# Kernel tuning notes

Measured on AMD Instinct MI355X. Metric: run time of the kernel, lower is better.

Reference implementation:

```python
import jax, jax.numpy as jnp
import numpy as np

DIM = 768
ALL_KEY_DIM = 768
NUM_HEADS = 12
HEAD_DIM = DIM // NUM_HEADS
SCALE = HEAD_DIM ** -0.5


def setup_inputs() -> dict:
    key = jax.random.key(0)
    ks = jax.random.split(key, 8)
    B, N = 8, 1024
    s = 0.02
    return {
        "x": jax.random.normal(ks[0], (B, N, DIM), dtype=jnp.float32),
        "Wq": jax.random.normal(ks[1], (ALL_KEY_DIM, DIM), dtype=jnp.float32) * s,
        "Wk": jax.random.normal(ks[2], (ALL_KEY_DIM, DIM), dtype=jnp.float32) * s,
        "Wv": jax.random.normal(ks[3], (DIM, DIM), dtype=jnp.float32) * s,
        "bv": jnp.zeros((DIM,), dtype=jnp.float32),
        "Wmix": jax.random.normal(ks[4], (NUM_HEADS, ALL_KEY_DIM), dtype=jnp.float32) * s,
        "Wcb": jax.random.normal(ks[5], (NUM_HEADS, DIM), dtype=jnp.float32) * s,
        "Wproj": jax.random.normal(ks[6], (DIM, DIM), dtype=jnp.float32) * s,
        "bproj": jnp.zeros((DIM,), dtype=jnp.float32),
    }


def reference(x, Wq, Wk, Wv, bv, Wmix, Wcb, Wproj, bproj):
    B, N, C = x.shape
    H, Dh = NUM_HEADS, C // NUM_HEADS
    q_shared = x @ Wq.T                      # [B,N,Dk]
    k = x @ Wk.T                             # [B,N,Dk]
    v = (x @ Wv.T + bv).reshape(B, N, H, Dh).transpose(0, 2, 1, 3)  # [B,H,N,Dh]
    # per-head mixed query: q[b,h,n,d] = q_shared[b,n,d] * Wmix[h,d]
    q = jnp.einsum('bnd,hd->bhnd', q_shared, Wmix)
    # shared-key scores + content bias broadcast over query positions
    scores = jnp.einsum('bhnd,bmd->bhnm', q, k)          # [B,H,N,N]
    content_bias = jnp.einsum('bmd,hd->bhm', x, Wcb)     # [B,H,N]
    attn = jax.nn.softmax((scores + content_bias[:, :, None, :]) * SCALE, axis=-1)
    out = jnp.einsum('bhnm,bhmd->bhnd', attn, v)         # [B,H,N,Dh]
    out = out.transpose(0, 2, 1, 3).reshape(B, N, C)
    return out @ Wproj.T + bproj
```

## Files before the change

### kernel.cpp

```cpp
#include <hip/hip_runtime.h>
#include <stdint.h>

typedef unsigned short u16;
typedef unsigned char u8;
typedef unsigned long long u64;
typedef __attribute__((ext_vector_type(8))) short bf16x8;
typedef __attribute__((ext_vector_type(4))) float f32x4;
typedef __attribute__((ext_vector_type(16))) float f32x16;

#define KLOG2E 0.18033688011112043f
#define QSCL 184.66496523378732f
#define SINV 0.0001220703125f
#define EXP2F(x) __builtin_amdgcn_exp2f(x)
#define WAITV(n) asm volatile("s_waitcnt vmcnt(" #n ")" ::: "memory")

__device__ __forceinline__ u16 f2bf(float f) {
  union { float f; unsigned u; } v; v.f = f;
  unsigned r = v.u + 0x7fffu + ((v.u >> 16) & 1u);
  return (u16)(r >> 16);
}
__device__ __forceinline__ float bf2f(u16 u) {
  union { unsigned u; float f; } v; v.u = ((unsigned)u) << 16;
  return v.f;
}
__device__ __forceinline__ u8 f2fp8(float f) {
  return (u8)(__builtin_amdgcn_cvt_pk_fp8_f32(f, f, 0, false) & 0xFF);
}

__device__ __forceinline__ void gload16(const void* g, void* l) {
  __builtin_amdgcn_global_load_lds(
      (const __attribute__((address_space(1))) unsigned int*)g,
      (__attribute__((address_space(3))) unsigned int*)l, 16, 0, 0);
}

__global__ void cvt_f32_bf16(const float4* __restrict__ s, uint2* __restrict__ d, int n4) {
  int i = blockIdx.x * blockDim.x + threadIdx.x;
  int stride = gridDim.x * blockDim.x;
  for (; i < n4; i += stride) {
    float4 v = s[i];
    uint2 o;
    o.x = (unsigned)f2bf(v.x) | ((unsigned)f2bf(v.y) << 16);
    o.y = (unsigned)f2bf(v.z) | ((unsigned)f2bf(v.w) << 16);
    d[i] = o;
  }
}

template <int MODE>
__global__ __launch_bounds__(256, 2) void gemm_bt(
    const u16* __restrict__ A, const u16* __restrict__ Bm,
    void* __restrict__ Cp, void* __restrict__ Cp2,
    const float* __restrict__ bias, int ldc) {
  __shared__ u16 Ab[128 * 32];
  __shared__ u16 Bb[128 * 32];
  const int tid = threadIdx.x;
  const int l = tid & 63, w = tid >> 6;
  const int g = l >> 4, l15 = l & 15;
  const int wr = w >> 1, wc = w & 1;
  const int rowbase = blockIdx.y * 128, colbase = blockIdx.x * 128;

  f32x4 acc[4][4] = {};
  const char* Abase = (const char*)A + (size_t)rowbase * 1536;
  const char* Bbase = (const char*)Bm + (size_t)colbase * 1536;

  for (int kk = 0; kk < 768; kk += 32) {
    __syncthreads();
#pragma unroll
    for (int p = 0; p < 2; ++p) {
      int o = p * 4096 + w * 1024 + l * 16;
      int row = o >> 6, cb = o & 63;
      gload16(Abase + (size_t)row * 1536 + kk * 2 + cb, &Ab[(p * 4096 + w * 1024) / 2]);
      gload16(Bbase + (size_t)row * 1536 + kk * 2 + cb, &Bb[(p * 4096 + w * 1024) / 2]);
    }
    __syncthreads();
    bf16x8 af[4], bfr[4];
#pragma unroll
    for (int i = 0; i < 4; ++i) {
      af[i] = *(const bf16x8*)&Ab[(wr * 64 + i * 16 + l15) * 32 + g * 8];
      bfr[i] = *(const bf16x8*)&Bb[(wc * 64 + i * 16 + l15) * 32 + g * 8];
    }
#pragma unroll
    for (int mi = 0; mi < 4; ++mi)
#pragma unroll
      for (int ni = 0; ni < 4; ++ni)
        acc[mi][ni] = __builtin_amdgcn_mfma_f32_16x16x32_bf16(af[mi], bfr[ni], acc[mi][ni], 0, 0, 0);
  }

#pragma unroll
  for (int mi = 0; mi < 4; ++mi)
#pragma unroll
    for (int ni = 0; ni < 4; ++ni)
#pragma unroll
      for (int r = 0; r < 4; ++r) {
        int row = rowbase + wr * 64 + mi * 16 + g * 4 + r;
        int col = colbase + wc * 64 + ni * 16 + l15;
        float v = acc[mi][ni][r];
        if (MODE == 0) {
          if (col < 768) {
            ((u16*)Cp)[(size_t)row * 768 + col] = f2bf(v);
          } else {
            int d = col - 768;
            int dp = d ^ ((((row) >> 3) & 1) << 3);
            ((u8*)Cp2)[(size_t)row * 768 + dp] = f2fp8(v * 8.0f);
          }
        } else if (MODE == 2) {
          ((float*)Cp)[(size_t)row * ldc + col] = v + bias[col];
        } else {
          int b = col >> 10, nn = col & 1023;
          if (row < 768) {
            ((u16*)Cp)[(size_t)b * 786432 + (size_t)row * 1024 + nn] = f2bf(v + bias[row]);
          } else if (row < 780) {
            ((float*)Cp2)[(size_t)b * 12288 + (size_t)(row - 768) * 1024 + nn] = v * KLOG2E;
          }
        }
      }
}

__global__ __launch_bounds__(256, 2) void attn10(
    const u16* __restrict__ Qb,
    const u8* __restrict__ Kf8,
    const u16* __restrict__ vT,
    const float* __restrict__ cb,
    const float* __restrict__ Wmix,
    u16* __restrict__ OH)
{
  __shared__ u8 Kb[3][8192];
  __shared__ u16 Vb[2][4096];
  __shared__ float cbL[1024];

  const int gid = blockIdx.x;
  const int b = gid & 7;
  const int within = gid >> 3;
  const int h = within % 12, qt = within / 12;
  const int tid = threadIdx.x;
  const int lane = tid & 63, w = tid >> 6;
  const int c = lane & 31, hi = lane >> 5;
  const int hsw = (c >> 3) & 1;

  const u8* Ksrc = Kf8 + (size_t)b * 786432;
  const char* Vsrc = (const char*)vT + (size_t)(b * 12 + h) * 131072;
  const float* cbp = cb + (size_t)(b * 12 + h) * 1024;

  long qreg[48];
  {
    const u16* qrow = Qb + ((size_t)b * 1024 + qt * 128 + w * 32 + c) * 768;
    const float* wmh = Wmix + h * 768;
#pragma unroll
    for (int D = 0; D < 48; ++D) {
      int off = D * 16 + hi * 8;
      bf16x8 qv = *(const bf16x8*)(qrow + off);
      float4 w0 = *(const float4*)(wmh + off);
      float4 w1 = *(const float4*)(wmh + off + 4);
      float q0 = bf2f((u16)qv[0]) * (w0.x * QSCL);
      float q1 = bf2f((u16)qv[1]) * (w0.y * QSCL);
      float q2 = bf2f((u16)qv[2]) * (w0.z * QSCL);
      float q3 = bf2f((u16)qv[3]) * (w0.w * QSCL);
      float q4 = bf2f((u16)qv[4]) * (w1.x * QSCL);
      float q5 = bf2f((u16)qv[5]) * (w1.y * QSCL);
      float q6 = bf2f((u16)qv[6]) * (w1.z * QSCL);
      float q7 = bf2f((u16)qv[7]) * (w1.w * QSCL);
      int a = __builtin_amdgcn_cvt_pk_fp8_f32(q0, q1, 0, false);
      a = __builtin_amdgcn_cvt_pk_fp8_f32(q2, q3, a, true);
      int b2 = __builtin_amdgcn_cvt_pk_fp8_f32(q4, q5, 0, false);
      b2 = __builtin_amdgcn_cvt_pk_fp8_f32(q6, q7, b2, true);
      qreg[D] = (long)(((u64)(unsigned)b2 << 32) | (u64)(unsigned)a);
    }
  }

  auto STK = [&](int kt2, int ch2, int buf) {
#pragma unroll
    for (int p4 = 0; p4 < 2; ++p4) {
      int o = p4 * 4096 + tid * 16;
      int row = o >> 7, t = (o >> 4) & 7;
      gload16(Ksrc + (size_t)(kt2 * 64 + row) * 768 + ch2 * 128 + ((t ^ (row & 7)) * 16),
              (char*)Kb[buf] + o);
    }
  };
  auto STV = [&](int kt2, int buf) {
#pragma unroll
    for (int p4 = 0; p4 < 2; ++p4) {
      int o = p4 * 4096 + tid * 16;
      int row = o >> 7, t = (o >> 4) & 7;
      gload16(Vsrc + (size_t)row * 2048 + kt2 * 128 + ((t ^ (row & 7)) * 16),
              (char*)Vb[buf] + o);
    }
  };

  {
    int o = tid * 16;
    gload16((const char*)cbp + o, (char*)cbL + o);
  }
  STK(0, 0, 0);
  STK(0, 1, 1);
  STV(0, 0);
  WAITV(0);
  __builtin_amdgcn_s_barrier();

  float m_run = -1e30f, lpart = 0.f;
  f32x16 oac0 = {}, oac1 = {};

#pragma unroll 1
  for (int kt = 0; kt < 16; ++kt) {
    f32x16 sa0 = {}, sa1 = {};
#pragma unroll
    for (int ch = 0; ch < 6; ++ch) {
      if (ch == 1 && kt < 15) STV(kt + 1, (kt + 1) & 1);
      if (ch <= 3) STK(kt, ch + 2, (ch + 2) % 3);
      else if (kt < 15) STK(kt + 1, ch - 4, (ch + 2) % 3);

      __builtin_amdgcn_s_setprio(1);
      const u8* kb0 = Kb[ch % 3] + c * 128 + ((hi ^ hsw) * 8);
#pragma unroll
      for (int s = 0; s < 8; ++s) {
        const u8* pK = kb0 + ((s ^ (c & 7)) << 4);
        long k0 = *(const long*)pK;
        long k1 = *(const long*)(pK + 4096);
        sa0 = __builtin_amdgcn_mfma_f32_32x32x16_fp8_fp8(k0, qreg[ch * 8 + s], sa0, 0, 0, 0);
        sa1 = __builtin_amdgcn_mfma_f32_32x32x16_fp8_fp8(k1, qreg[ch * 8 + s], sa1, 0, 0, 0);
      }
      __builtin_amdgcn_s_setprio(0);

      if (ch == 0) { WAITV(2); }
      else if (ch == 1) { if (kt < 15) { WAITV(4); } else { WAITV(2); } }
      else if (ch == 4 || ch == 5) { if (kt < 15) { WAITV(2); } else { WAITV(0); } }
      else { WAITV(2); }
      __builtin_amdgcn_s_barrier();
    }

    float cb0[16], cb1[16];
#pragma unroll
    for (int j = 0; j < 4; ++j) {
      float4 t0 = *(const float4*)&cbL[kt * 64 + 8 * j + 4 * hi];
      float4 t1 = *(const float4*)&cbL[kt * 64 + 32 + 8 * j + 4 * hi];
      cb0[4 * j] = t0.x; cb0[4 * j + 1] = t0.y; cb0[4 * j + 2] = t0.z; cb0[4 * j + 3] = t0.w;
      cb1[4 * j] = t1.x; cb1[4 * j + 1] = t1.y; cb1[4 * j + 2] = t1.z; cb1[4 * j + 3] = t1.w;
    }
    float pmax = -1e30f;
#pragma unroll
    for (int u = 0; u < 16; ++u) {
      sa0[u] = fmaf(sa0[u], SINV, cb0[u]);
      sa1[u] = fmaf(sa1[u], SINV, cb1[u]);
      pmax = fmaxf(pmax, fmaxf(sa0[u], sa1[u]));
    }
    pmax = fmaxf(pmax, __shfl_xor(pmax, 32));
    if (__ballot(pmax > m_run)) {
      float mnew = fmaxf(m_run, pmax);
      float alpha = EXP2F(m_run - mnew);
      lpart *= alpha;
      oac0 *= alpha;
      oac1 *= alpha;
      m_run = mnew;
    }
    float rs = 0.f;
#pragma unroll
    for (int u = 0; u < 16; ++u) {
      sa0[u] = EXP2F(sa0[u] - m_run); rs += sa0[u];
      sa1[u] = EXP2F(sa1[u] - m_run); rs += sa1[u];
    }
    rs += __shfl_xor(rs, 32);
    lpart += rs;

    const char* vb = (const char*)Vb[kt & 1];
#pragma unroll
    for (int kg = 0; kg < 2; ++kg) {
#pragma unroll
      for (int win = 0; win < 2; ++win) {
        float p0, p1, p2, p3, p4, p5, p6, p7;
        if (kg == 0) {
          p0 = sa0[win * 8 + 0]; p1 = sa0[win * 8 + 1]; p2 = sa0[win * 8 + 2]; p3 = sa0[win * 8 + 3];
          p4 = sa0[win * 8 + 4]; p5 = sa0[win * 8 + 5]; p6 = sa0[win * 8 + 6]; p7 = sa0[win * 8 + 7];
        } else {
          p0 = sa1[win * 8 + 0]; p1 = sa1[win * 8 + 1]; p2 = sa1[win * 8 + 2]; p3 = sa1[win * 8 + 3];
          p4 = sa1[win * 8 + 4]; p5 = sa1[win * 8 + 5]; p6 = sa1[win * 8 + 6]; p7 = sa1[win * 8 + 7];
        }
        unsigned xw, yw, zw, tw;
        asm("v_cvt_pk_bf16_f32 %0, %1, %2" : "=v"(xw) : "v"(p0), "v"(p1));
        asm("v_cvt_pk_bf16_f32 %0, %1, %2" : "=v"(yw) : "v"(p2), "v"(p3));
        asm("v_cvt_pk_bf16_f32 %0, %1, %2" : "=v"(zw) : "v"(p4), "v"(p5));
        asm("v_cvt_pk_bf16_f32 %0, %1, %2" : "=v"(tw) : "v"(p6), "v"(p7));
        asm volatile("v_permlane32_swap_b32 %0, %1" : "+v"(xw), "+v"(zw));
        asm volatile("v_permlane32_swap_b32 %0, %1" : "+v"(yw), "+v"(tw));
        union { unsigned u[4]; bf16x8 v; } bu;
        bu.u[0] = xw; bu.u[1] = yw; bu.u[2] = zw; bu.u[3] = tw;
#pragma unroll
        for (int dg = 0; dg < 2; ++dg) {
          int rd = dg * 32 + c;
          int sv = kg * 4 + win * 2 + hi;
          bf16x8 vf = *(const bf16x8*)(vb + rd * 128 + ((sv ^ (rd & 7)) * 16));
          if (dg == 0)
            oac0 = __builtin_amdgcn_mfma_f32_32x32x16_bf16(vf, bu.v, oac0, 0, 0, 0);
          else
            oac1 = __builtin_amdgcn_mfma_f32_32x32x16_bf16(vf, bu.v, oac1, 0, 0, 0);
        }
      }
    }
  }

  float rdiv = 1.f / lpart;
  int n = qt * 128 + w * 32 + c;
  size_t nrow = ((size_t)b * 1024 + n) * 768 + h * 64;
#pragma unroll
  for (int dg = 0; dg < 2; ++dg)
#pragma unroll
    for (int j = 0; j < 4; ++j) {
      f32x16 oo = dg == 0 ? oac0 : oac1;
      u64 pk = (u64)f2bf(oo[4 * j + 0] * rdiv) |
               ((u64)f2bf(oo[4 * j + 1] * rdiv) << 16) |
               ((u64)f2bf(oo[4 * j + 2] * rdiv) << 32) |
               ((u64)f2bf(oo[4 * j + 3] * rdiv) << 48);
      *(u64*)&OH[nrow + dg * 32 + 8 * j + 4 * hi] = pk;
    }
}

static inline int cvtblocks(int n4) {
  int nb = (n4 + 255) / 256;
  return nb > 2048 ? 2048 : nb;
}

extern "C" void kernel_launch(void* const* d_in, const int* in_sizes, int n_in,
                              void* d_out, int out_size, void* d_ws, size_t ws_size,
                              hipStream_t stream) {
  (void)in_sizes; (void)n_in; (void)out_size; (void)ws_size;
  const float* x = (const float*)d_in[0];
  const float* Wq = (const float*)d_in[1];
  const float* Wk = (const float*)d_in[2];
  const float* Wv = (const float*)d_in[3];
  const float* bv = (const float*)d_in[4];
  const float* Wmix = (const float*)d_in[5];
  const float* Wcb = (const float*)d_in[6];
  const float* Wproj = (const float*)d_in[7];
  const float* bproj = (const float*)d_in[8];
  float* out = (float*)d_out;

  char* ws = (char*)d_ws;
  u16* xbf = (u16*)(ws);
  u16* Wqk = (u16*)(ws + 12582912);
  u16* Wvcb = (u16*)(ws + 14942208);
  u16* Wpj = (u16*)(ws + 16318464);
  u16* Qb = (u16*)(ws + 17498112);
  u8* Kf8 = (u8*)(ws + 30081024);
  u16* vT = (u16*)(ws + 36372480);
  float* cbb = (float*)(ws + 48955392);
  u16* OH = (u16*)(ws + 49348608);

  cvt_f32_bf16<<<cvtblocks(1572864), 256, 0, stream>>>((const float4*)x, (uint2*)xbf, 1572864);
  cvt_f32_bf16<<<cvtblocks(147456), 256, 0, stream>>>((const float4*)Wq, (uint2*)Wqk, 147456);
  cvt_f32_bf16<<<cvtblocks(147456), 256, 0, stream>>>((const float4*)Wk, (uint2*)(Wqk + 589824), 147456);
  cvt_f32_bf16<<<cvtblocks(147456), 256, 0, stream>>>((const float4*)Wv, (uint2*)Wvcb, 147456);
  cvt_f32_bf16<<<cvtblocks(2304), 256, 0, stream>>>((const float4*)Wcb, (uint2*)(Wvcb + 589824), 2304);
  cvt_f32_bf16<<<cvtblocks(147456), 256, 0, stream>>>((const float4*)Wproj, (uint2*)Wpj, 147456);

  gemm_bt<0><<<dim3(12, 64), 256, 0, stream>>>(xbf, Wqk, Qb, Kf8, nullptr, 0);
  gemm_bt<1><<<dim3(64, 7), 256, 0, stream>>>(Wvcb, xbf, vT, cbb, bv, 0);
  attn10<<<dim3(768), 256, 0, stream>>>(Qb, Kf8, vT, cbb, Wmix, OH);
  gemm_bt<2><<<dim3(6, 64), 256, 0, stream>>>(OH, Wpj, out, nullptr, bproj, 768);
}
```

Before: 279.6 us.

## Use 32x32x64 scaled FP8 MFMA for QK scores with double-buffered 256-byte K chunks

Replaces the 32x32x16 fp8 MFMA in the QK^T score loop with the gfx950 mfma_scale 32x32x64 f8f6f4 instruction, so each instruction covers four times the reduction depth. K staging moves from a triple buffer of 128-byte-wide chunks to a double buffer of 256-byte chunks with a new XOR swizzle. Query packing becomes i32x8 registers, and Q preparation is moved after the first K/V loads are issued so it overlaps them. The K layout swizzle in the projection GEMM epilogue is dropped. Waits now sit before each compute step rather than after it, which exposes more load latency with only two buffers.

```diff
diff --git a/kernel.cpp b/kernel.cpp
--- a/kernel.cpp
+++ b/kernel.cpp
@@ -7,6 +7,7 @@
 typedef __attribute__((ext_vector_type(8))) short bf16x8;
 typedef __attribute__((ext_vector_type(4))) float f32x4;
 typedef __attribute__((ext_vector_type(16))) float f32x16;
+typedef __attribute__((ext_vector_type(8))) int i32x8;
 
 #define KLOG2E 0.18033688011112043f
 #define QSCL 184.66496523378732f
@@ -98,9 +99,7 @@
           if (col < 768) {
             ((u16*)Cp)[(size_t)row * 768 + col] = f2bf(v);
           } else {
-            int d = col - 768;
-            int dp = d ^ ((((row) >> 3) & 1) << 3);
-            ((u8*)Cp2)[(size_t)row * 768 + dp] = f2fp8(v * 8.0f);
+            ((u8*)Cp2)[(size_t)row * 768 + (col - 768)] = f2fp8(v * 8.0f);
           }
         } else if (MODE == 2) {
           ((float*)Cp)[(size_t)row * ldc + col] = v + bias[col];
@@ -115,7 +114,7 @@
       }
 }
 
-__global__ __launch_bounds__(256, 2) void attn10(
+__global__ __launch_bounds__(256, 2) void attn11(
     const u16* __restrict__ Qb,
     const u8* __restrict__ Kf8,
     const u16* __restrict__ vT,
@@ -123,7 +122,7 @@
     const float* __restrict__ Wmix,
     u16* __restrict__ OH)
 {
-  __shared__ u8 Kb[3][8192];
+  __shared__ u8 Kb[2][16384];
   __shared__ u16 Vb[2][4096];
   __shared__ float cbL[1024];
 
@@ -134,44 +133,18 @@
   const int tid = threadIdx.x;
   const int lane = tid & 63, w = tid >> 6;
   const int c = lane & 31, hi = lane >> 5;
-  const int hsw = (c >> 3) & 1;
 
   const u8* Ksrc = Kf8 + (size_t)b * 786432;
   const char* Vsrc = (const char*)vT + (size_t)(b * 12 + h) * 131072;
   const float* cbp = cb + (size_t)(b * 12 + h) * 1024;
 
-  long qreg[48];
-  {
-    const u16* qrow = Qb + ((size_t)b * 1024 + qt * 128 + w * 32 + c) * 768;
-    const float* wmh = Wmix + h * 768;
-#pragma unroll
-    for (int D = 0; D < 48; ++D) {
-      int off = D * 16 + hi * 8;
-      bf16x8 qv = *(const bf16x8*)(qrow + off);
-      float4 w0 = *(const float4*)(wmh + off);
-      float4 w1 = *(const float4*)(wmh + off + 4);
-      float q0 = bf2f((u16)qv[0]) * (w0.x * QSCL);
-      float q1 = bf2f((u16)qv[1]) * (w0.y * QSCL);
-      float q2 = bf2f((u16)qv[2]) * (w0.z * QSCL);
-      float q3 = bf2f((u16)qv[3]) * (w0.w * QSCL);
-      float q4 = bf2f((u16)qv[4]) * (w1.x * QSCL);
-      float q5 = bf2f((u16)qv[5]) * (w1.y * QSCL);
-      float q6 = bf2f((u16)qv[6]) * (w1.z * QSCL);
-      float q7 = bf2f((u16)qv[7]) * (w1.w * QSCL);
-      int a = __builtin_amdgcn_cvt_pk_fp8_f32(q0, q1, 0, false);
-      a = __builtin_amdgcn_cvt_pk_fp8_f32(q2, q3, a, true);
-      int b2 = __builtin_amdgcn_cvt_pk_fp8_f32(q4, q5, 0, false);
-      b2 = __builtin_amdgcn_cvt_pk_fp8_f32(q6, q7, b2, true);
-      qreg[D] = (long)(((u64)(unsigned)b2 << 32) | (u64)(unsigned)a);
-    }
-  }
-
-  auto STK = [&](int kt2, int ch2, int buf) {
-#pragma unroll
-    for (int p4 = 0; p4 < 2; ++p4) {
+  auto STK = [&](int kt2, int p2, int buf) {
+#pragma unroll
+    for (int p4 = 0; p4 < 4; ++p4) {
       int o = p4 * 4096 + tid * 16;
-      int row = o >> 7, t = (o >> 4) & 7;
-      gload16(Ksrc + (size_t)(kt2 * 64 + row) * 768 + ch2 * 128 + ((t ^ (row & 7)) * 16),
+      int row = o >> 8;
+      int t = (o >> 4) & 15;
+      gload16(Ksrc + (size_t)(kt2 * 64 + row) * 768 + p2 * 256 + ((t ^ (row & 15)) * 16),
               (char*)Kb[buf] + o);
     }
   };
@@ -190,10 +163,39 @@
     gload16((const char*)cbp + o, (char*)cbL + o);
   }
   STK(0, 0, 0);
-  STK(0, 1, 1);
   STV(0, 0);
-  WAITV(0);
-  __builtin_amdgcn_s_barrier();
+
+  i32x8 qreg[12];
+  {
+    const u16* qrow = Qb + ((size_t)b * 1024 + qt * 128 + w * 32 + c) * 768;
+    const float* wmh = Wmix + h * 768;
+#pragma unroll
+    for (int D = 0; D < 12; ++D) {
+      i32x8 qq;
+#pragma unroll
+      for (int j = 0; j < 4; ++j) {
+        int off = D * 64 + hi * 32 + j * 8;
+        bf16x8 qv = *(const bf16x8*)(qrow + off);
+        float4 w0 = *(const float4*)(wmh + off);
+        float4 w1 = *(const float4*)(wmh + off + 4);
+        float q0 = bf2f((u16)qv[0]) * (w0.x * QSCL);
+        float q1 = bf2f((u16)qv[1]) * (w0.y * QSCL);
+        float q2 = bf2f((u16)qv[2]) * (w0.z * QSCL);
+        float q3 = bf2f((u16)qv[3]) * (w0.w * QSCL);
+        float q4 = bf2f((u16)qv[4]) * (w1.x * QSCL);
+        float q5 = bf2f((u16)qv[5]) * (w1.y * QSCL);
+        float q6 = bf2f((u16)qv[6]) * (w1.z * QSCL);
+        float q7 = bf2f((u16)qv[7]) * (w1.w * QSCL);
+        int a = __builtin_amdgcn_cvt_pk_fp8_f32(q0, q1, 0, false);
+        a = __builtin_amdgcn_cvt_pk_fp8_f32(q2, q3, a, true);
+        int b2 = __builtin_amdgcn_cvt_pk_fp8_f32(q4, q5, 0, false);
+        b2 = __builtin_amdgcn_cvt_pk_fp8_f32(q6, q7, b2, true);
+        qq[2 * j] = a;
+        qq[2 * j + 1] = b2;
+      }
+      qreg[D] = qq;
+    }
+  }
 
   float m_run = -1e30f, lpart = 0.f;
   f32x16 oac0 = {}, oac1 = {};
@@ -202,43 +204,51 @@
   for (int kt = 0; kt < 16; ++kt) {
     f32x16 sa0 = {}, sa1 = {};
 #pragma unroll
-    for (int ch = 0; ch < 6; ++ch) {
-      if (ch == 1 && kt < 15) STV(kt + 1, (kt + 1) & 1);
-      if (ch <= 3) STK(kt, ch + 2, (ch + 2) % 3);
-      else if (kt < 15) STK(kt + 1, ch - 4, (ch + 2) % 3);
+    for (int p = 0; p < 3; ++p) {
+      const int cp = kt * 3 + p;
+      if (p < 2) STK(kt, p + 1, (cp + 1) & 1);
+      else if (kt < 15) STK(kt + 1, 0, (cp + 1) & 1);
+      if (p == 1 && kt < 15) STV(kt + 1, (kt + 1) & 1);
+
+      if (p == 0) { if (kt == 0) { WAITV(6); } else { WAITV(4); } }
+      else if (p == 1) { if (kt < 15) { WAITV(6); } else { WAITV(4); } }
+      else { if (kt < 15) { WAITV(6); } else { WAITV(0); } }
+      __builtin_amdgcn_s_barrier();
 
       __builtin_amdgcn_s_setprio(1);
-      const u8* kb0 = Kb[ch % 3] + c * 128 + ((hi ^ hsw) * 8);
-#pragma unroll
-      for (int s = 0; s < 8; ++s) {
-        const u8* pK = kb0 + ((s ^ (c & 7)) << 4);
-        long k0 = *(const long*)pK;
-        long k1 = *(const long*)(pK + 4096);
-        sa0 = __builtin_amdgcn_mfma_f32_32x32x16_fp8_fp8(k0, qreg[ch * 8 + s], sa0, 0, 0, 0);
-        sa1 = __builtin_amdgcn_mfma_f32_32x32x16_fp8_fp8(k1, qreg[ch * 8 + s], sa1, 0, 0, 0);
+      const u8* kbuf = Kb[cp & 1];
+#pragma unroll
+      for (int dd = 0; dd < 4; ++dd) {
+        const int D = p * 4 + dd;
+#pragma unroll
+        for (int kg = 0; kg < 2; ++kg) {
+          int r = kg * 32 + c;
+          int sb = dd * 4 + hi * 2;
+          const u8* kb = kbuf + r * 256;
+          uint4 lo = *(const uint4*)(kb + (((sb) ^ (r & 15)) << 4));
+          uint4 h4 = *(const uint4*)(kb + (((sb + 1) ^ (r & 15)) << 4));
+          i32x8 af;
+          af[0] = (int)lo.x; af[1] = (int)lo.y; af[2] = (int)lo.z; af[3] = (int)lo.w;
+          af[4] = (int)h4.x; af[5] = (int)h4.y; af[6] = (int)h4.z; af[7] = (int)h4.w;
+          if (kg == 0)
+            sa0 = __builtin_amdgcn_mfma_scale_f32_32x32x64_f8f6f4(
+                af, qreg[D], sa0, 0, 0, 0, 127, 0, 127);
+          else
+            sa1 = __builtin_amdgcn_mfma_scale_f32_32x32x64_f8f6f4(
+                af, qreg[D], sa1, 0, 0, 0, 127, 0, 127);
+        }
       }
       __builtin_amdgcn_s_setprio(0);
-
-      if (ch == 0) { WAITV(2); }
-      else if (ch == 1) { if (kt < 15) { WAITV(4); } else { WAITV(2); } }
-      else if (ch == 4 || ch == 5) { if (kt < 15) { WAITV(2); } else { WAITV(0); } }
-      else { WAITV(2); }
       __builtin_amdgcn_s_barrier();
     }
 
-    float cb0[16], cb1[16];
-#pragma unroll
-    for (int j = 0; j < 4; ++j) {
-      float4 t0 = *(const float4*)&cbL[kt * 64 + 8 * j + 4 * hi];
-      float4 t1 = *(const float4*)&cbL[kt * 64 + 32 + 8 * j + 4 * hi];
-      cb0[4 * j] = t0.x; cb0[4 * j + 1] = t0.y; cb0[4 * j + 2] = t0.z; cb0[4 * j + 3] = t0.w;
-      cb1[4 * j] = t1.x; cb1[4 * j + 1] = t1.y; cb1[4 * j + 2] = t1.z; cb1[4 * j + 3] = t1.w;
-    }
     float pmax = -1e30f;
 #pragma unroll
     for (int u = 0; u < 16; ++u) {
-      sa0[u] = fmaf(sa0[u], SINV, cb0[u]);
-      sa1[u] = fmaf(sa1[u], SINV, cb1[u]);
+      float c0 = cbL[kt * 64 + ((u & 3) + 8 * (u >> 2) + 4 * hi)];
+      float c1 = cbL[kt * 64 + 32 + ((u & 3) + 8 * (u >> 2) + 4 * hi)];
+      sa0[u] = fmaf(sa0[u], SINV, c0);
+      sa1[u] = fmaf(sa1[u], SINV, c1);
       pmax = fmaxf(pmax, fmaxf(sa0[u], sa1[u]));
     }
     pmax = fmaxf(pmax, __shfl_xor(pmax, 32));
@@ -351,6 +361,6 @@
 
   gemm_bt<0><<<dim3(12, 64), 256, 0, stream>>>(xbf, Wqk, Qb, Kf8, nullptr, 0);
   gemm_bt<1><<<dim3(64, 7), 256, 0, stream>>>(Wvcb, xbf, vT, cbb, bv, 0);
-  attn10<<<dim3(768), 256, 0, stream>>>(Qb, Kf8, vT, cbb, Wmix, OH);
+  attn11<<<dim3(768), 256, 0, stream>>>(Qb, Kf8, vT, cbb, Wmix, OH);
   gemm_bt<2><<<dim3(6, 64), 256, 0, stream>>>(OH, Wpj, out, nullptr, bproj, 768);
 }
```

Result: slower. 344.6 us (+23.3%).

## Split attention key tiles across two warp groups with split-softmax merge

Applied to the files above, without the earlier changes.

The attention kernel now uses 512 threads per block: each query warp is paired with a second warp, and each of the two processes half of every 64-key tile. Their partial softmax max, sum and output accumulators are merged through shared memory at the end. Global-to-LDS loads are spread over more threads, and the first tile loads are issued before the Q register setup so that the setup overlaps them. This aims to raise wave occupancy and latency hiding. In exchange, Q is loaded and converted twice, the final merge needs an extra reduction with two barriers, and the launch bounds ask for high occupancy, which may cap registers and cause spills of the 48-entry Q register array.

```diff
diff --git a/kernel.cpp b/kernel.cpp
--- a/kernel.cpp
+++ b/kernel.cpp
@@ -31,6 +31,11 @@
   __builtin_amdgcn_global_load_lds(
       (const __attribute__((address_space(1))) unsigned int*)g,
       (__attribute__((address_space(3))) unsigned int*)l, 16, 0, 0);
+}
+__device__ __forceinline__ void gload4(const void* g, void* l) {
+  __builtin_amdgcn_global_load_lds(
+      (const __attribute__((address_space(1))) unsigned int*)g,
+      (__attribute__((address_space(3))) unsigned int*)l, 4, 0, 0);
 }
 
 __global__ void cvt_f32_bf16(const float4* __restrict__ s, uint2* __restrict__ d, int n4) {
@@ -115,7 +120,7 @@
       }
 }
 
-__global__ __launch_bounds__(256, 2) void attn10(
+__global__ __launch_bounds__(512, 6) void attn12(
     const u16* __restrict__ Qb,
     const u8* __restrict__ Kf8,
     const u16* __restrict__ vT,
@@ -123,9 +128,11 @@
     const float* __restrict__ Wmix,
     u16* __restrict__ OH)
 {
-  __shared__ u8 Kb[3][8192];
-  __shared__ u16 Vb[2][4096];
-  __shared__ float cbL[1024];
+  __shared__ __align__(16) u8 SM[49152];
+  u8* KbB = SM;
+  u8* VbB = SM + 24576;
+  float* cbL = (float*)(SM + 40960);
+  float* MxL = (float*)(SM + 45056);
 
   const int gid = blockIdx.x;
   const int b = gid & 7;
@@ -134,15 +141,35 @@
   const int tid = threadIdx.x;
   const int lane = tid & 63, w = tid >> 6;
   const int c = lane & 31, hi = lane >> 5;
+  const int p = w & 3, e = w >> 2;
   const int hsw = (c >> 3) & 1;
 
   const u8* Ksrc = Kf8 + (size_t)b * 786432;
   const char* Vsrc = (const char*)vT + (size_t)(b * 12 + h) * 131072;
   const float* cbp = cb + (size_t)(b * 12 + h) * 1024;
 
+  auto STK = [&](int kt2, int ch2, int buf) {
+    int o = tid * 16;
+    int row = o >> 7, t = (o >> 4) & 7;
+    gload16(Ksrc + (size_t)(kt2 * 64 + row) * 768 + ch2 * 128 + ((t ^ (row & 7)) * 16),
+            KbB + buf * 8192 + o);
+  };
+  auto STV = [&](int kt2, int buf) {
+    int o = tid * 16;
+    int row = o >> 7, t = (o >> 4) & 7;
+    gload16(Vsrc + (size_t)row * 2048 + kt2 * 128 + ((t ^ (row & 7)) * 16),
+            VbB + buf * 8192 + o);
+  };
+
+  gload4(cbp + tid, cbL + ((tid >> 6) << 6));
+  gload4(cbp + 512 + tid, cbL + 512 + ((tid >> 6) << 6));
+  STK(0, 0, 0);
+  STV(0, 0);
+  STK(0, 1, 1);
+
   long qreg[48];
   {
-    const u16* qrow = Qb + ((size_t)b * 1024 + qt * 128 + w * 32 + c) * 768;
+    const u16* qrow = Qb + ((size_t)b * 1024 + qt * 128 + p * 32 + c) * 768;
     const float* wmh = Wmix + h * 768;
 #pragma unroll
     for (int D = 0; D < 48; ++D) {
@@ -166,33 +193,7 @@
     }
   }
 
-  auto STK = [&](int kt2, int ch2, int buf) {
-#pragma unroll
-    for (int p4 = 0; p4 < 2; ++p4) {
-      int o = p4 * 4096 + tid * 16;
-      int row = o >> 7, t = (o >> 4) & 7;
-      gload16(Ksrc + (size_t)(kt2 * 64 + row) * 768 + ch2 * 128 + ((t ^ (row & 7)) * 16),
-              (char*)Kb[buf] + o);
-    }
-  };
-  auto STV = [&](int kt2, int buf) {
-#pragma unroll
-    for (int p4 = 0; p4 < 2; ++p4) {
-      int o = p4 * 4096 + tid * 16;
-      int row = o >> 7, t = (o >> 4) & 7;
-      gload16(Vsrc + (size_t)row * 2048 + kt2 * 128 + ((t ^ (row & 7)) * 16),
-              (char*)Vb[buf] + o);
-    }
-  };
-
-  {
-    int o = tid * 16;
-    gload16((const char*)cbp + o, (char*)cbL + o);
-  }
-  STK(0, 0, 0);
-  STK(0, 1, 1);
-  STV(0, 0);
-  WAITV(0);
+  WAITV(2);
   __builtin_amdgcn_s_barrier();
 
   float m_run = -1e30f, lpart = 0.f;
@@ -200,46 +201,44 @@
 
 #pragma unroll 1
   for (int kt = 0; kt < 16; ++kt) {
-    f32x16 sa0 = {}, sa1 = {};
+    f32x16 sa = {};
 #pragma unroll
     for (int ch = 0; ch < 6; ++ch) {
-      if (ch == 1 && kt < 15) STV(kt + 1, (kt + 1) & 1);
-      if (ch <= 3) STK(kt, ch + 2, (ch + 2) % 3);
-      else if (kt < 15) STK(kt + 1, ch - 4, (ch + 2) % 3);
+      if (ch <= 3) {
+        STK(kt, ch + 2, (ch + 2) % 3);
+      } else if (ch == 4) {
+        if (kt < 15) STK(kt + 1, 0, 0);
+      } else {
+        if (kt < 15) { STK(kt + 1, 1, 1); STV(kt + 1, (kt + 1) & 1); }
+      }
 
       __builtin_amdgcn_s_setprio(1);
-      const u8* kb0 = Kb[ch % 3] + c * 128 + ((hi ^ hsw) * 8);
+      const u8* kb0 = KbB + (ch % 3) * 8192 + e * 4096 + c * 128 + ((hi ^ hsw) * 8);
 #pragma unroll
       for (int s = 0; s < 8; ++s) {
-        const u8* pK = kb0 + ((s ^ (c & 7)) << 4);
-        long k0 = *(const long*)pK;
-        long k1 = *(const long*)(pK + 4096);
-        sa0 = __builtin_amdgcn_mfma_f32_32x32x16_fp8_fp8(k0, qreg[ch * 8 + s], sa0, 0, 0, 0);
-        sa1 = __builtin_amdgcn_mfma_f32_32x32x16_fp8_fp8(k1, qreg[ch * 8 + s], sa1, 0, 0, 0);
+        long k0 = *(const long*)(kb0 + ((s ^ (c & 7)) << 4));
+        sa = __builtin_amdgcn_mfma_f32_32x32x16_fp8_fp8(k0, qreg[ch * 8 + s], sa, 0, 0, 0);
       }
       __builtin_amdgcn_s_setprio(0);
 
-      if (ch == 0) { WAITV(2); }
-      else if (ch == 1) { if (kt < 15) { WAITV(4); } else { WAITV(2); } }
-      else if (ch == 4 || ch == 5) { if (kt < 15) { WAITV(2); } else { WAITV(0); } }
-      else { WAITV(2); }
+      if (ch == 0) { if (kt == 0) { WAITV(1); } else { WAITV(2); } }
+      else if (ch <= 3) { WAITV(1); }
+      else if (ch == 4) { if (kt < 15) { WAITV(1); } else { WAITV(0); } }
+      else { if (kt < 15) { WAITV(2); } }
       __builtin_amdgcn_s_barrier();
     }
 
-    float cb0[16], cb1[16];
+    float cbq[16];
 #pragma unroll
     for (int j = 0; j < 4; ++j) {
-      float4 t0 = *(const float4*)&cbL[kt * 64 + 8 * j + 4 * hi];
-      float4 t1 = *(const float4*)&cbL[kt * 64 + 32 + 8 * j + 4 * hi];
-      cb0[4 * j] = t0.x; cb0[4 * j + 1] = t0.y; cb0[4 * j + 2] = t0.z; cb0[4 * j + 3] = t0.w;
-      cb1[4 * j] = t1.x; cb1[4 * j + 1] = t1.y; cb1[4 * j + 2] = t1.z; cb1[4 * j + 3] = t1.w;
+      float4 t = *(const float4*)&cbL[kt * 64 + e * 32 + 8 * j + 4 * hi];
+      cbq[4 * j] = t.x; cbq[4 * j + 1] = t.y; cbq[4 * j + 2] = t.z; cbq[4 * j + 3] = t.w;
     }
     float pmax = -1e30f;
 #pragma unroll
     for (int u = 0; u < 16; ++u) {
-      sa0[u] = fmaf(sa0[u], SINV, cb0[u]);
-      sa1[u] = fmaf(sa1[u], SINV, cb1[u]);
-      pmax = fmaxf(pmax, fmaxf(sa0[u], sa1[u]));
+      sa[u] = fmaf(sa[u], SINV, cbq[u]);
+      pmax = fmaxf(pmax, sa[u]);
     }
     pmax = fmaxf(pmax, __shfl_xor(pmax, 32));
     if (__ballot(pmax > m_run)) {
@@ -253,62 +252,80 @@
     float rs = 0.f;
 #pragma unroll
     for (int u = 0; u < 16; ++u) {
-      sa0[u] = EXP2F(sa0[u] - m_run); rs += sa0[u];
-      sa1[u] = EXP2F(sa1[u] - m_run); rs += sa1[u];
+      sa[u] = EXP2F(sa[u] - m_run);
+      rs += sa[u];
     }
     rs += __shfl_xor(rs, 32);
     lpart += rs;
 
-    const char* vb = (const char*)Vb[kt & 1];
-#pragma unroll
-    for (int kg = 0; kg < 2; ++kg) {
-#pragma unroll
-      for (int win = 0; win < 2; ++win) {
-        float p0, p1, p2, p3, p4, p5, p6, p7;
-        if (kg == 0) {
-          p0 = sa0[win * 8 + 0]; p1 = sa0[win * 8 + 1]; p2 = sa0[win * 8 + 2]; p3 = sa0[win * 8 + 3];
-          p4 = sa0[win * 8 + 4]; p5 = sa0[win * 8 + 5]; p6 = sa0[win * 8 + 6]; p7 = sa0[win * 8 + 7];
-        } else {
-          p0 = sa1[win * 8 + 0]; p1 = sa1[win * 8 + 1]; p2 = sa1[win * 8 + 2]; p3 = sa1[win * 8 + 3];
-          p4 = sa1[win * 8 + 4]; p5 = sa1[win * 8 + 5]; p6 = sa1[win * 8 + 6]; p7 = sa1[win * 8 + 7];
-        }
-        unsigned xw, yw, zw, tw;
-        asm("v_cvt_pk_bf16_f32 %0, %1, %2" : "=v"(xw) : "v"(p0), "v"(p1));
-        asm("v_cvt_pk_bf16_f32 %0, %1, %2" : "=v"(yw) : "v"(p2), "v"(p3));
-        asm("v_cvt_pk_bf16_f32 %0, %1, %2" : "=v"(zw) : "v"(p4), "v"(p5));
-        asm("v_cvt_pk_bf16_f32 %0, %1, %2" : "=v"(tw) : "v"(p6), "v"(p7));
-        asm volatile("v_permlane32_swap_b32 %0, %1" : "+v"(xw), "+v"(zw));
-        asm volatile("v_permlane32_swap_b32 %0, %1" : "+v"(yw), "+v"(tw));
-        union { unsigned u[4]; bf16x8 v; } bu;
-        bu.u[0] = xw; bu.u[1] = yw; bu.u[2] = zw; bu.u[3] = tw;
-#pragma unroll
-        for (int dg = 0; dg < 2; ++dg) {
-          int rd = dg * 32 + c;
-          int sv = kg * 4 + win * 2 + hi;
-          bf16x8 vf = *(const bf16x8*)(vb + rd * 128 + ((sv ^ (rd & 7)) * 16));
-          if (dg == 0)
-            oac0 = __builtin_amdgcn_mfma_f32_32x32x16_bf16(vf, bu.v, oac0, 0, 0, 0);
-          else
-            oac1 = __builtin_amdgcn_mfma_f32_32x32x16_bf16(vf, bu.v, oac1, 0, 0, 0);
-        }
+    const char* vb = (const char*)VbB + (kt & 1) * 8192;
+#pragma unroll
+    for (int win = 0; win < 2; ++win) {
+      unsigned xw, yw, zw, tw;
+      asm("v_cvt_pk_bf16_f32 %0, %1, %2" : "=v"(xw) : "v"(sa[win * 8 + 0]), "v"(sa[win * 8 + 1]));
+      asm("v_cvt_pk_bf16_f32 %0, %1, %2" : "=v"(yw) : "v"(sa[win * 8 + 2]), "v"(sa[win * 8 + 3]));
+      asm("v_cvt_pk_bf16_f32 %0, %1, %2" : "=v"(zw) : "v"(sa[win * 8 + 4]), "v"(sa[win * 8 + 5]));
+      asm("v_cvt_pk_bf16_f32 %0, %1, %2" : "=v"(tw) : "v"(sa[win * 8 + 6]), "v"(sa[win * 8 + 7]));
+      asm volatile("v_permlane32_swap_b32 %0, %1" : "+v"(xw), "+v"(zw));
+      asm volatile("v_permlane32_swap_b32 %0, %1" : "+v"(yw), "+v"(tw));
+      union { unsigned u[4]; bf16x8 v; } bu;
+      bu.u[0] = xw; bu.u[1] = yw; bu.u[2] = zw; bu.u[3] = tw;
+#pragma unroll
+      for (int dg = 0; dg < 2; ++dg) {
+        int rd = dg * 32 + c;
+        int sv = e * 4 + win * 2 + hi;
+        bf16x8 vf = *(const bf16x8*)(vb + rd * 128 + ((sv ^ (rd & 7)) * 16));
+        if (dg == 0)
+          oac0 = __builtin_amdgcn_mfma_f32_32x32x16_bf16(vf, bu.v, oac0, 0, 0, 0);
+        else
+          oac1 = __builtin_amdgcn_mfma_f32_32x32x16_bf16(vf, bu.v, oac1, 0, 0, 0);
       }
     }
   }
 
-  float rdiv = 1.f / lpart;
-  int n = qt * 128 + w * 32 + c;
-  size_t nrow = ((size_t)b * 1024 + n) * 768 + h * 64;
-#pragma unroll
-  for (int dg = 0; dg < 2; ++dg)
+  MxL[((p * 2 + e) * 64 + lane) * 2 + 0] = m_run;
+  MxL[((p * 2 + e) * 64 + lane) * 2 + 1] = lpart;
+  __syncthreads();
+  float m_o = MxL[((p * 2 + (e ^ 1)) * 64 + lane) * 2 + 0];
+  float l_o = MxL[((p * 2 + (e ^ 1)) * 64 + lane) * 2 + 1];
+  float mstar = fmaxf(m_run, m_o);
+  float sc = EXP2F(m_run - mstar);
+  float lfull = lpart * sc + l_o * EXP2F(m_o - mstar);
+
+  float4* MG = (float4*)SM;
+  if (e == 1) {
 #pragma unroll
     for (int j = 0; j < 4; ++j) {
-      f32x16 oo = dg == 0 ? oac0 : oac1;
-      u64 pk = (u64)f2bf(oo[4 * j + 0] * rdiv) |
-               ((u64)f2bf(oo[4 * j + 1] * rdiv) << 16) |
-               ((u64)f2bf(oo[4 * j + 2] * rdiv) << 32) |
-               ((u64)f2bf(oo[4 * j + 3] * rdiv) << 48);
-      *(u64*)&OH[nrow + dg * 32 + 8 * j + 4 * hi] = pk;
-    }
+      float4 t0, t1;
+      t0.x = oac0[4 * j] * sc;     t0.y = oac0[4 * j + 1] * sc;
+      t0.z = oac0[4 * j + 2] * sc; t0.w = oac0[4 * j + 3] * sc;
+      t1.x = oac1[4 * j] * sc;     t1.y = oac1[4 * j + 1] * sc;
+      t1.z = oac1[4 * j + 2] * sc; t1.w = oac1[4 * j + 3] * sc;
+      MG[j * 256 + p * 64 + lane] = t0;
+      MG[(4 + j) * 256 + p * 64 + lane] = t1;
+    }
+  }
+  __syncthreads();
+  if (e == 0) {
+    float rdiv = 1.f / lfull;
+    int n = qt * 128 + p * 32 + c;
+    size_t nrow = ((size_t)b * 1024 + n) * 768 + h * 64;
+#pragma unroll
+    for (int j = 0; j < 4; ++j) {
+      float4 r0 = MG[j * 256 + p * 64 + lane];
+      float4 r1 = MG[(4 + j) * 256 + p * 64 + lane];
+      u64 pk0 = (u64)f2bf((oac0[4 * j + 0] * sc + r0.x) * rdiv) |
+                ((u64)f2bf((oac0[4 * j + 1] * sc + r0.y) * rdiv) << 16) |
+                ((u64)f2bf((oac0[4 * j + 2] * sc + r0.z) * rdiv) << 32) |
+                ((u64)f2bf((oac0[4 * j + 3] * sc + r0.w) * rdiv) << 48);
+      u64 pk1 = (u64)f2bf((oac1[4 * j + 0] * sc + r1.x) * rdiv) |
+                ((u64)f2bf((oac1[4 * j + 1] * sc + r1.y) * rdiv) << 16) |
+                ((u64)f2bf((oac1[4 * j + 2] * sc + r1.z) * rdiv) << 32) |
+                ((u64)f2bf((oac1[4 * j + 3] * sc + r1.w) * rdiv) << 48);
+      *(u64*)&OH[nrow + 8 * j + 4 * hi] = pk0;
+      *(u64*)&OH[nrow + 32 + 8 * j + 4 * hi] = pk1;
+    }
+  }
 }
 
 static inline int cvtblocks(int n4) {
@@ -351,6 +368,6 @@
 
   gemm_bt<0><<<dim3(12, 64), 256, 0, stream>>>(xbf, Wqk, Qb, Kf8, nullptr, 0);
   gemm_bt<1><<<dim3(64, 7), 256, 0, stream>>>(Wvcb, xbf, vT, cbb, bv, 0);
-  attn10<<<dim3(768), 256, 0, stream>>>(Qb, Kf8, vT, cbb, Wmix, OH);
+  attn12<<<dim3(768), 512, 0, stream>>>(Qb, Kf8, vT, cbb, Wmix, OH);
   gemm_bt<2><<<dim3(6, 64), 256, 0, stream>>>(OH, Wpj, out, nullptr, bproj, 768);
 }
```

After: 556.1 us. +98.9%, slower.
